# Kernel tuning notes

Measured on AMD Instinct MI355X. Metric: run time of the kernel, lower is better.

Reference implementation:

```python
import jax, jax.numpy as jnp
import numpy as np

K = 16  # neighbors, incl. self


def setup_inputs() -> dict:
    key = jax.random.key(0)
    ks = jax.random.split(key, 16)
    N, C = 8192, 256  # points, channels (inter_channels == in_channels == C)
    s = 0.05
    inp = {
        'coords': jax.random.uniform(ks[0], (N, 3), dtype=jnp.float32) * 100.0,
        'feats': jax.random.normal(ks[1], (N, C), dtype=jnp.float32),
        'theta_w': jax.random.normal(ks[2], (C, C), dtype=jnp.float32) * s,
        'theta_b': jax.random.normal(ks[3], (C,), dtype=jnp.float32) * s,
        'phi_w': jax.random.normal(ks[4], (C, C), dtype=jnp.float32) * s,
        'phi_b': jax.random.normal(ks[5], (C,), dtype=jnp.float32) * s,
        'g_w': jax.random.normal(ks[6], (C, C), dtype=jnp.float32) * s,
        'g_b': jax.random.normal(ks[7], (C,), dtype=jnp.float32) * s,
        'pe1_w1': jax.random.normal(ks[8], (3, C), dtype=jnp.float32) * s,
        'pe1_b1': jax.random.normal(ks[9], (C,), dtype=jnp.float32) * s,
        'pe1_w2': jax.random.normal(ks[10], (C, C), dtype=jnp.float32) * s,
        'pe1_b2': jax.random.normal(ks[11], (C,), dtype=jnp.float32) * s,
        'W_w': jax.random.normal(ks[12], (C, C), dtype=jnp.float32) * s,
        'W_b': jax.random.normal(ks[13], (C,), dtype=jnp.float32) * s,
    }
    return inp


def reference(coords, feats, theta_w, theta_b, phi_w, phi_b, g_w, g_b,
              pe1_w1, pe1_b1, pe1_w2, pe1_b2, W_w, W_b):
    C = feats.shape[-1]
    # KNN (squared dists, includes self as nearest) == pytorch3d knn_points
    sq = jnp.sum(coords * coords, axis=-1)  # [N]
    d2 = sq[:, None] + sq[None, :] - 2.0 * (coords @ coords.T)  # [N,N]
    _, idx = jax.lax.top_k(-d2, K)  # [N,K] sorted by ascending distance

    nn_coords = coords[idx]            # [N,K,3] knn gather
    nn_feats = feats[idx]              # [N,K,C]

    theta_f = feats @ theta_w + theta_b          # [N,C]
    phi_f = nn_feats @ phi_w + phi_b             # [N,K,C]

    delta_coords = nn_coords - coords[:, None, :]  # [N,K,3]
    # pe1 MLP; NOTE: original code uses pe1 for both pe1 and pe2 (shared)
    pe = jax.nn.relu(delta_coords @ pe1_w1 + pe1_b1) @ pe1_w2 + pe1_b2  # [N,K,C]

    delta_features = (pe * (theta_f[:, None, :] - phi_f) + pe) / jnp.sqrt(jnp.float32(C))
    sim = jax.nn.softmax(delta_features, axis=1)  # softmax over K neighbors

    g_feats = nn_feats @ g_w + g_b               # [N,K,C]
    y = jnp.sum(sim * g_feats, axis=1)           # [N,C]

    # W (1x1 Minkowski conv == per-point linear) + residual
    return y @ W_w + W_b + feats
```

## Files before the change

### kernel.cpp

```cpp
#include <hip/hip_runtime.h>

typedef __bf16 bf16_t;
typedef bf16_t bf16x8 __attribute__((ext_vector_type(8)));
typedef bf16_t bf16x4 __attribute__((ext_vector_type(4)));
typedef bf16_t bf16x2 __attribute__((ext_vector_type(2)));
typedef float f32x4 __attribute__((ext_vector_type(4)));
typedef unsigned long long u64;

#define N_PTS 8192
#define C_DIM 256
#define K_NN 16

#define GRID_G    16
#define GRID_NC   (GRID_G * GRID_G * GRID_G)
#define GRID_CELL 6.25f
#define GRID_INV  0.16f

#define CAST_NBLK 2048
#define PREPW_NBLK 320
__global__ __launch_bounds__(256) void prep_kernel(
    const float* __restrict__ feats, bf16_t* __restrict__ fb,
    const float* __restrict__ w0, const float* __restrict__ w1,
    const float* __restrict__ w2, const float* __restrict__ w3,
    const float* __restrict__ w4, bf16_t* __restrict__ wt_base,
    int* __restrict__ cellCount, int* __restrict__ gcount) {
    const int b = blockIdx.x;
    const int t = threadIdx.x;

    if (b < CAST_NBLK) {
        int i = (b * 256 + t) * 4;
        float4 v = *(const float4*)(feats + i);
        bf16x4 o;
        o[0] = (bf16_t)v.x; o[1] = (bf16_t)v.y; o[2] = (bf16_t)v.z; o[3] = (bf16_t)v.w;
        *(bf16x4*)(fb + i) = o;
    } else if (b < CAST_NBLK + PREPW_NBLK) {
        int pb = b - CAST_NBLK;
        int m = pb >> 6;
        int bx = pb & 63;
        const float* src = (m == 0) ? w0 : (m == 1) ? w1 : (m == 2) ? w2 : (m == 3) ? w3 : w4;
        bf16_t* dst = wt_base + m * (C_DIM * C_DIM);
#pragma unroll
        for (int i = 0; i < 4; ++i) {
            int o = bx * 1024 + i * 256 + t;
            int tkb = o >> 9;
            int rem = o & 511;
            int lm = rem >> 5;
            int r = rem & 31;
            int k = (tkb & 7) * 32 + r;
            int n = (tkb >> 3) * 16 + lm;
            dst[o] = (bf16_t)src[k * C_DIM + n];
        }
    } else {
        int zb = b - CAST_NBLK - PREPW_NBLK;
        cellCount[zb * 256 + t] = 0;
        if (zb == 0 && t == 0) *gcount = 0;
    }
}

__global__ __launch_bounds__(256) void grid_count_kernel(const float* __restrict__ coords,
                                                         int* __restrict__ cellCount,
                                                         int* __restrict__ cid) {
    int i = blockIdx.x * 256 + threadIdx.x;
    float x = coords[3 * i + 0], y = coords[3 * i + 1], z = coords[3 * i + 2];
    int cx = (int)(x * GRID_INV); if (cx > GRID_G - 1) cx = GRID_G - 1;
    int cy = (int)(y * GRID_INV); if (cy > GRID_G - 1) cy = GRID_G - 1;
    int cz = (int)(z * GRID_INV); if (cz > GRID_G - 1) cz = GRID_G - 1;
    int c = (cx * GRID_G + cy) * GRID_G + cz;
    cid[i] = c;
    atomicAdd(&cellCount[c], 1);
}

__global__ __launch_bounds__(256) void grid_scan_kernel(const int* __restrict__ cellCount,
                                                        int* __restrict__ cellStart,
                                                        int* __restrict__ cellPtr) {
    __shared__ int part[256];
    int t = threadIdx.x;
    int base = t * 16;
    int v[16];
    int sum = 0;
#pragma unroll
    for (int i = 0; i < 16; ++i) { v[i] = cellCount[base + i]; sum += v[i]; }
    part[t] = sum;
    __syncthreads();
    for (int off = 1; off < 256; off <<= 1) {
        int x = (t >= off) ? part[t - off] : 0;
        __syncthreads();
        part[t] += x;
        __syncthreads();
    }
    int acc = part[t] - sum;
#pragma unroll
    for (int i = 0; i < 16; ++i) {
        cellStart[base + i] = acc;
        cellPtr[base + i] = acc;
        acc += v[i];
    }
    if (t == 255) cellStart[GRID_NC] = acc;
}

__global__ __launch_bounds__(256) void grid_scatter_kernel(
    const float* __restrict__ coords, const int* __restrict__ cid, int* __restrict__ cellPtr,
    float* __restrict__ sx, float* __restrict__ sy, float* __restrict__ sz,
    float* __restrict__ ssq, int* __restrict__ sidx) {
    int i = blockIdx.x * 256 + threadIdx.x;
    int c = cid[i];
    int pos = atomicAdd(&cellPtr[c], 1);
    float x = coords[3 * i + 0], y = coords[3 * i + 1], z = coords[3 * i + 2];
    sx[pos] = x; sy[pos] = y; sz[pos] = z;
    ssq[pos] = __fadd_rn(__fadd_rn(__fmul_rn(x, x), __fmul_rn(y, y)), __fmul_rn(z, z));
    sidx[pos] = i;
}

__global__ __launch_bounds__(256) void knn_grid_kernel(
    const float* __restrict__ coords, const int* __restrict__ cellStart,
    const float* __restrict__ sx, const float* __restrict__ sy,
    const float* __restrict__ sz, const float* __restrict__ ssq,
    const int* __restrict__ sidx,
    int* __restrict__ idx_out, int* __restrict__ glist, int* __restrict__ gcount) {
    const int tid = threadIdx.x;
    const int wave = tid >> 6, lane = tid & 63;
    const int q = blockIdx.x * 4 + wave;

    __shared__ int segBase[4][25];
    __shared__ int segPref[4][26];
    __shared__ u64 cand[4][256];
    __shared__ int cnt[4];

    if (lane == 0) cnt[wave] = 0;

    const float qx = coords[3 * q + 0], qy = coords[3 * q + 1], qz = coords[3 * q + 2];
    const float sqi = __fadd_rn(__fadd_rn(__fmul_rn(qx, qx), __fmul_rn(qy, qy)),
                                __fmul_rn(qz, qz));

    int cx = (int)(qx * GRID_INV); if (cx > GRID_G - 1) cx = GRID_G - 1;
    int cy = (int)(qy * GRID_INV); if (cy > GRID_G - 1) cy = GRID_G - 1;
    int cz = (int)(qz * GRID_INV); if (cz > GRID_G - 1) cz = GRID_G - 1;
    int wx0 = cx - 2; if (wx0 < 0) wx0 = 0;
    int wx1 = cx + 2; if (wx1 > GRID_G - 1) wx1 = GRID_G - 1;
    int wy0 = cy - 2; if (wy0 < 0) wy0 = 0;
    int wy1 = cy + 2; if (wy1 > GRID_G - 1) wy1 = GRID_G - 1;
    int wz0 = cz - 2; if (wz0 < 0) wz0 = 0;
    int wz1 = cz + 2; if (wz1 > GRID_G - 1) wz1 = GRID_G - 1;

    const float INF = __int_as_float(0x7f800000);
    float rc = INF;
    if (wx0 > 0)          rc = fminf(rc, qx - (float)wx0 * GRID_CELL);
    if (wx1 < GRID_G - 1) rc = fminf(rc, (float)(wx1 + 1) * GRID_CELL - qx);
    if (wy0 > 0)          rc = fminf(rc, qy - (float)wy0 * GRID_CELL);
    if (wy1 < GRID_G - 1) rc = fminf(rc, (float)(wy1 + 1) * GRID_CELL - qy);
    if (wz0 > 0)          rc = fminf(rc, qz - (float)wz0 * GRID_CELL);
    if (wz1 < GRID_G - 1) rc = fminf(rc, (float)(wz1 + 1) * GRID_CELL - qz);
    float rc2 = rc * rc * 0.9999f;

    int nx = wx1 - wx0 + 1, nyc = wy1 - wy0 + 1;
    int ns = nx * nyc;
    if (lane < ns) {
        int scx = wx0 + lane / nyc;
        int scy = wy0 + lane % nyc;
        int b = (scx * GRID_G + scy) * GRID_G;
        int s0 = cellStart[b + wz0];
        int s1 = cellStart[b + wz1 + 1];
        segBase[wave][lane] = s0;
        segPref[wave][lane] = s1 - s0;
    }
    __syncthreads();
    if (lane == 0) {
        int acc = 0;
        for (int s = 0; s < ns; ++s) { int l = segPref[wave][s]; segPref[wave][s] = acc; acc += l; }
        segPref[wave][ns] = acc;
    }
    __syncthreads();

    const int M = segPref[wave][ns];
    bool flag = (M < K_NN);

    float lmin = INF;
    {
        int s = 0;
        for (int t = lane; t < M; t += 64) {
            while (t >= segPref[wave][s + 1]) ++s;
            int pos = segBase[wave][s] + (t - segPref[wave][s]);
            float x = sx[pos], y = sy[pos], z = sz[pos], sj = ssq[pos];
            float dot = __fmaf_rn(z, qz, __fmaf_rn(y, qy, __fmul_rn(x, qx)));
            float d2 = __fsub_rn(__fadd_rn(sqi, sj), __fmul_rn(2.0f, dot));
            lmin = fminf(lmin, d2);
        }
    }
    float g = fminf(lmin, __shfl_xor(lmin, 1));
    g = fminf(g, __shfl_xor(g, 2));
    float tau = fmaxf(g, __shfl_xor(g, 4));
    tau = fmaxf(tau, __shfl_xor(tau, 8));
    tau = fmaxf(tau, __shfl_xor(tau, 16));
    tau = fmaxf(tau, __shfl_xor(tau, 32));

    {
        int s = 0;
        for (int t = lane; t < M; t += 64) {
            while (t >= segPref[wave][s + 1]) ++s;
            int pos = segBase[wave][s] + (t - segPref[wave][s]);
            float x = sx[pos], y = sy[pos], z = sz[pos], sj = ssq[pos];
            float dot = __fmaf_rn(z, qz, __fmaf_rn(y, qy, __fmul_rn(x, qx)));
            float d2 = __fsub_rn(__fadd_rn(sqi, sj), __fmul_rn(2.0f, dot));
            if (d2 <= tau) {
                unsigned u = __float_as_uint(d2);
                u = (u & 0x80000000u) ? ~u : (u | 0x80000000u);
                int slot = atomicAdd(&cnt[wave], 1);
                if (slot < 256)
                    cand[wave][slot] = (((u64)u) << 32) | (unsigned)sidx[pos];
            }
        }
    }
    __syncthreads();

    int m = cnt[wave];
    if (m > 256) { flag = true; m = 256; }
    u64 k0 = ~0ull, k1 = ~0ull, k2 = ~0ull, k3 = ~0ull;
    if (lane < m) k0 = cand[wave][lane];
    if (lane + 64 < m) k1 = cand[wave][lane + 64];
    if (lane + 128 < m) k2 = cand[wave][lane + 128];
    if (lane + 192 < m) k3 = cand[wave][lane + 192];
    u64 lm2 = k0; int li = 0;
    if (k1 < lm2) { lm2 = k1; li = 1; }
    if (k2 < lm2) { lm2 = k2; li = 2; }
    if (k3 < lm2) { lm2 = k3; li = 3; }
    int keep = 0;
    u64 last = ~0ull;
#pragma unroll 1
    for (int r = 0; r < 16; ++r) {
        u64 w = lm2;
#pragma unroll
        for (int off = 1; off < 64; off <<= 1) {
            u64 o = __shfl_xor(w, off);
            w = (o < w) ? o : w;
        }
        if (lane == r) keep = (int)(unsigned)(w & 0xffffffffull);
        last = w;
        if (lm2 == w) {
            if (li == 0) k0 = ~0ull;
            else if (li == 1) k1 = ~0ull;
            else if (li == 2) k2 = ~0ull;
            else k3 = ~0ull;
            lm2 = k0; li = 0;
            if (k1 < lm2) { lm2 = k1; li = 1; }
            if (k2 < lm2) { lm2 = k2; li = 2; }
            if (k3 < lm2) { lm2 = k3; li = 3; }
        }
    }

    if (!flag) {
        unsigned ou = (unsigned)(last >> 32);
        unsigned db = (ou & 0x80000000u) ? (ou ^ 0x80000000u) : ~ou;
        float d16 = __uint_as_float(db);
        if (d16 >= rc2) flag = true;
    }
    if (flag && lane == 0) {
        int sl = atomicAdd(gcount, 1);
        glist[sl] = q;
    }
    if (lane < 16) idx_out[q * K_NN + lane] = keep;
}

__global__ __launch_bounds__(256) void knn_fallback_kernel(const float* __restrict__ coords,
                                                           const int* __restrict__ glist,
                                                           const int* __restrict__ gcount,
                                                           int* __restrict__ idx_out) {
    const int count = *gcount;
    const int n0 = blockIdx.x * 4;
    if (n0 >= count) return;

    const int tid = threadIdx.x;
    const int wave = tid >> 6, lane = tid & 63;
    __shared__ float red16[4][16];
    __shared__ u64 cand[4][256];
    __shared__ int cnt[4];
    __shared__ int qids[4];

    if (tid < 4) {
        cnt[tid] = 0;
        int slot = n0 + tid;
        qids[tid] = glist[slot < count ? slot : count - 1];
    }
    __syncthreads();

    float qx[4], qy[4], qz[4], sqi[4];
#pragma unroll
    for (int q = 0; q < 4; ++q) {
        int id = qids[q];
        qx[q] = coords[3 * id + 0];
        qy[q] = coords[3 * id + 1];
        qz[q] = coords[3 * id + 2];
        sqi[q] = __fadd_rn(__fadd_rn(__fmul_rn(qx[q], qx[q]), __fmul_rn(qy[q], qy[q])),
                           __fmul_rn(qz[q], qz[q]));
    }

    const float INF = __int_as_float(0x7f800000);
    const float* cp = coords + tid * 96;

    float lmin[4] = {INF, INF, INF, INF};
#pragma unroll
    for (int c = 0; c < 4; ++c) {
        float buf[24];
#pragma unroll
        for (int v = 0; v < 6; ++v)
            *(float4*)(buf + v * 4) = *(const float4*)(cp + c * 24 + v * 4);
#pragma unroll
        for (int p = 0; p < 8; ++p) {
            float x = buf[3 * p + 0], y = buf[3 * p + 1], z = buf[3 * p + 2];
            float sqj = __fadd_rn(__fadd_rn(__fmul_rn(x, x), __fmul_rn(y, y)),
                                  __fmul_rn(z, z));
#pragma unroll
            for (int q = 0; q < 4; ++q) {
                float dot = __fmaf_rn(z, qz[q], __fmaf_rn(y, qy[q], __fmul_rn(x, qx[q])));
                float d2 = __fsub_rn(__fadd_rn(sqi[q], sqj), __fmul_rn(2.0f, dot));
                lmin[q] = fminf(lmin[q], d2);
            }
        }
    }

#pragma unroll
    for (int q = 0; q < 4; ++q) {
        float g = lmin[q];
        g = fminf(g, __shfl_xor(g, 1));
        g = fminf(g, __shfl_xor(g, 2));
        g = fminf(g, __shfl_xor(g, 4));
        g = fminf(g, __shfl_xor(g, 8));
        if ((lane & 15) == 0) red16[q][wave * 4 + (lane >> 4)] = g;
    }
    __syncthreads();

    float tau[4];
#pragma unroll
    for (int q = 0; q < 4; ++q) {
        float t = red16[q][0];
#pragma unroll
        for (int i = 1; i < 16; ++i) t = fmaxf(t, red16[q][i]);
        tau[q] = t;
    }

#pragma unroll
    for (int c = 0; c < 4; ++c) {
        float buf[24];
#pragma unroll
        for (int v = 0; v < 6; ++v)
            *(float4*)(buf + v * 4) = *(const float4*)(cp + c * 24 + v * 4);
#pragma unroll
        for (int p = 0; p < 8; ++p) {
            float x = buf[3 * p + 0], y = buf[3 * p + 1], z = buf[3 * p + 2];
            float sqj = __fadd_rn(__fadd_rn(__fmul_rn(x, x), __fmul_rn(y, y)),
                                  __fmul_rn(z, z));
            int j = tid * 32 + c * 8 + p;
#pragma unroll
            for (int q = 0; q < 4; ++q) {
                float dot = __fmaf_rn(z, qz[q], __fmaf_rn(y, qy[q], __fmul_rn(x, qx[q])));
                float d2 = __fsub_rn(__fadd_rn(sqi[q], sqj), __fmul_rn(2.0f, dot));
                if (d2 <= tau[q]) {
                    unsigned u = __float_as_uint(d2);
                    u = (u & 0x80000000u) ? ~u : (u | 0x80000000u);
                    int slot = atomicAdd(&cnt[q], 1);
                    if (slot < 256)
                        cand[q][slot] = (((u64)u) << 32) | (unsigned)j;
                }
            }
        }
    }
    __syncthreads();

    int m = cnt[wave]; if (m > 256) m = 256;
    u64 k0 = ~0ull, k1 = ~0ull, k2 = ~0ull, k3 = ~0ull;
    if (lane < m) k0 = cand[wave][lane];
    if (lane + 64 < m) k1 = cand[wave][lane + 64];
    if (lane + 128 < m) k2 = cand[wave][lane + 128];
    if (lane + 192 < m) k3 = cand[wave][lane + 192];
    u64 lm2 = k0; int li = 0;
    if (k1 < lm2) { lm2 = k1; li = 1; }
    if (k2 < lm2) { lm2 = k2; li = 2; }
    if (k3 < lm2) { lm2 = k3; li = 3; }
    int keep = 0;
#pragma unroll 1
    for (int r = 0; r < 16; ++r) {
        u64 w = lm2;
#pragma unroll
        for (int off = 1; off < 64; off <<= 1) {
            u64 o = __shfl_xor(w, off);
            w = (o < w) ? o : w;
        }
        if (lane == r) keep = (int)(unsigned)(w & 0xffffffffull);
        if (lm2 == w) {
            if (li == 0) k0 = ~0ull;
            else if (li == 1) k1 = ~0ull;
            else if (li == 2) k2 = ~0ull;
            else k3 = ~0ull;
            lm2 = k0; li = 0;
            if (k1 < lm2) { lm2 = k1; li = 1; }
            if (k2 < lm2) { lm2 = k2; li = 2; }
            if (k3 < lm2) { lm2 = k3; li = 3; }
        }
    }
    if (lane < 16) idx_out[qids[wave] * K_NN + lane] = keep;
}

__global__ __launch_bounds__(256, 2) void proj_kernel(
    const bf16_t* __restrict__ fb, const bf16_t* __restrict__ wt_base,
    const float* __restrict__ tb, const float* __restrict__ pb, const float* __restrict__ gb,
    float* __restrict__ T, bf16_t* __restrict__ PG) {
    const int sel = blockIdx.y;
    const bf16_t* Wt = wt_base + sel * (C_DIM * C_DIM);
    const float* bias = (sel == 0) ? tb : (sel == 1) ? pb : gb;
    const int wave = threadIdx.x >> 6, lane = threadIdx.x & 63;
    const int q = lane >> 4, lm = lane & 15;
    const int m0 = blockIdx.x * 64;

    bf16x8 bfr[4][8];
#pragma unroll
    for (int ti = 0; ti < 4; ++ti)
#pragma unroll
        for (int kb = 0; kb < 8; ++kb)
            bfr[ti][kb] = *(const bf16x8*)(Wt + (((wave * 4 + ti) * 8 + kb) << 9) + lm * 32 + q * 8);

    float bv[4];
#pragma unroll
    for (int ti = 0; ti < 4; ++ti) bv[ti] = bias[(wave * 4 + ti) * 16 + lm];

#pragma unroll
    for (int p = 0; p < 4; ++p) {
        const bf16_t* arow = fb + (m0 + p * 16 + lm) * C_DIM + q * 8;
        bf16x8 a[8];
#pragma unroll
        for (int kb = 0; kb < 8; ++kb) a[kb] = *(const bf16x8*)(arow + kb * 32);
        f32x4 acc[4];
#pragma unroll
        for (int ti = 0; ti < 4; ++ti) acc[ti] = (f32x4){0.f, 0.f, 0.f, 0.f};
#pragma unroll
        for (int ti = 0; ti < 4; ++ti)
#pragma unroll
            for (int kb = 0; kb < 8; ++kb)
                acc[ti] = __builtin_amdgcn_mfma_f32_16x16x32_bf16(a[kb], bfr[ti][kb], acc[ti], 0, 0, 0);

#pragma unroll
        for (int ti = 0; ti < 4; ++ti) {
            int c = (wave * 4 + ti) * 16 + lm;
#pragma unroll
            for (int r = 0; r < 4; ++r) {
                float v = acc[ti][r] + bv[ti];
                int off = (m0 + p * 16 + q * 4 + r) * C_DIM + c;
                if (sel == 0) T[off] = v;
                else if (sel == 1) PG[2 * off] = (bf16_t)v;
                else PG[2 * off + 1] = (bf16_t)v;
            }
        }
    }
}

#define HPAD 264
#define P_BLK 8
#define HROWS (P_BLK * 16)
__global__ __launch_bounds__(256, 3) void pe2_fused_kernel(
    const float* __restrict__ coords, const int* __restrict__ idx,
    const float* __restrict__ T, const bf16_t* __restrict__ PG,
    const float* __restrict__ w1, const float* __restrict__ b1, const float* __restrict__ b2,
    const bf16_t* __restrict__ Wt2, bf16_t* __restrict__ yb) {
    __shared__ __align__(16) bf16_t hbuf[2][16 * HPAD];
    __shared__ float dxyz[HROWS][3];
    __shared__ int idxl[HROWS];
    const int tid = threadIdx.x;
    const int p0 = blockIdx.x * P_BLK;
    const int half = blockIdx.y;
    const int wave = tid >> 6, lane = tid & 63;
    const int q = lane >> 4, lm = lane & 15;

    bf16x8 bfr[2][8];
#pragma unroll
    for (int ti = 0; ti < 2; ++ti)
#pragma unroll
        for (int kb = 0; kb < 8; ++kb)
            bfr[ti][kb] = *(const bf16x8*)(Wt2 + ((((half * 8 + wave * 2 + ti) * 8 + kb)) << 9) + lm * 32 + q * 8);
    float b2c[2];
#pragma unroll
    for (int ti = 0; ti < 2; ++ti) b2c[ti] = b2[(half * 8 + wave * 2 + ti) * 16 + lm];

    if (tid < HROWS) {
        int n = p0 + (tid >> 4);
        int j = idx[n * K_NN + (tid & 15)];
        idxl[tid] = j;
        dxyz[tid][0] = coords[3 * j + 0] - coords[3 * n + 0];
        dxyz[tid][1] = coords[3 * j + 1] - coords[3 * n + 1];
        dxyz[tid][2] = coords[3 * j + 2] - coords[3 * n + 2];
    }
    __syncthreads();

    const float wx = w1[tid], wy = w1[C_DIM + tid], wz = w1[2 * C_DIM + tid], bb = b1[tid];

    {
#pragma unroll
        for (int r = 0; r < 16; ++r) {
            float pre = dxyz[r][0] * wx + dxyz[r][1] * wy + dxyz[r][2] * wz + bb;
            hbuf[0][r * HPAD + tid] = (bf16_t)fmaxf(pre, 0.0f);
        }
    }
    __syncthreads();

#pragma unroll 1
    for (int lp = 0; lp < P_BLK; ++lp) {
        const int n = p0 + lp;
        const int cur = lp & 1;

        int jr[4];
#pragma unroll
        for (int r = 0; r < 4; ++r) jr[r] = idxl[lp * 16 + q * 4 + r];
        bf16x2 pg[2][4];
        float Tn[2];
#pragma unroll
        for (int ti = 0; ti < 2; ++ti) {
            int c = (half * 8 + wave * 2 + ti) * 16 + lm;
            Tn[ti] = T[n * C_DIM + c];
#pragma unroll
            for (int r = 0; r < 4; ++r)
                pg[ti][r] = *(const bf16x2*)(PG + 2 * (jr[r] * C_DIM + c));
        }

        if (lp + 1 < P_BLK) {
            int rb = (lp + 1) * 16;
#pragma unroll
            for (int r = 0; r < 16; ++r) {
                float pre = dxyz[rb + r][0] * wx + dxyz[rb + r][1] * wy + dxyz[rb + r][2] * wz + bb;
                hbuf[cur ^ 1][r * HPAD + tid] = (bf16_t)fmaxf(pre, 0.0f);
            }
        }

        const bf16_t* hrow = &hbuf[cur][lm * HPAD + q * 8];
        f32x4 acc[2];
        acc[0] = (f32x4){0.f, 0.f, 0.f, 0.f};
        acc[1] = (f32x4){0.f, 0.f, 0.f, 0.f};
#pragma unroll
        for (int kb = 0; kb < 8; ++kb) {
            bf16x8 a = *(const bf16x8*)(hrow + kb * 32);
            acc[0] = __builtin_amdgcn_mfma_f32_16x16x32_bf16(a, bfr[0][kb], acc[0], 0, 0, 0);
            acc[1] = __builtin_amdgcn_mfma_f32_16x16x32_bf16(a, bfr[1][kb], acc[1], 0, 0, 0);
        }

#pragma unroll
        for (int ti = 0; ti < 2; ++ti) {
            int c = (half * 8 + wave * 2 + ti) * 16 + lm;
            float df[4];
#pragma unroll
            for (int r = 0; r < 4; ++r) {
                float pe = acc[ti][r] + b2c[ti];
                df[r] = (pe * (Tn[ti] - (float)pg[ti][r][0]) + pe) * 0.0625f;
            }
            float mx = fmaxf(fmaxf(df[0], df[1]), fmaxf(df[2], df[3]));
            mx = fmaxf(mx, __shfl_xor(mx, 16));
            mx = fmaxf(mx, __shfl_xor(mx, 32));
            float e[4], s = 0.f;
#pragma unroll
            for (int r = 0; r < 4; ++r) { e[r] = __expf(df[r] - mx); s += e[r]; }
            s += __shfl_xor(s, 16);
            s += __shfl_xor(s, 32);
            float inv = 1.0f / s;
            float y = 0.f;
#pragma unroll
            for (int r = 0; r < 4; ++r) y += e[r] * inv * (float)pg[ti][r][1];
            y += __shfl_xor(y, 16);
            y += __shfl_xor(y, 32);
            if (q == 0) yb[n * C_DIM + c] = (bf16_t)y;
        }
        __syncthreads();
    }
}

__global__ __launch_bounds__(256, 2) void final_kernel(
    const bf16_t* __restrict__ yb, const bf16_t* __restrict__ Wt,
    const float* __restrict__ Wb, const float* __restrict__ feats,
    float* __restrict__ out) {
    const int wave = threadIdx.x >> 6, lane = threadIdx.x & 63;
    const int q = lane >> 4, lm = lane & 15;
    const int m0 = blockIdx.x * 64;

    bf16x8 bfr[4][8];
#pragma unroll
    for (int ti = 0; ti < 4; ++ti)
#pragma unroll
        for (int kb = 0; kb < 8; ++kb)
            bfr[ti][kb] = *(const bf16x8*)(Wt + (((wave * 4 + ti) * 8 + kb) << 9) + lm * 32 + q * 8);
    float bv[4];
#pragma unroll
    for (int ti = 0; ti < 4; ++ti) bv[ti] = Wb[(wave * 4 + ti) * 16 + lm];

#pragma unroll
    for (int p = 0; p < 4; ++p) {
        const bf16_t* arow = yb + (m0 + p * 16 + lm) * C_DIM + q * 8;
        bf16x8 a[8];
#pragma unroll
        for (int kb = 0; kb < 8; ++kb) a[kb] = *(const bf16x8*)(arow + kb * 32);
        f32x4 acc[4];
#pragma unroll
        for (int ti = 0; ti < 4; ++ti) acc[ti] = (f32x4){0.f, 0.f, 0.f, 0.f};
#pragma unroll
        for (int ti = 0; ti < 4; ++ti)
#pragma unroll
            for (int kb = 0; kb < 8; ++kb)
                acc[ti] = __builtin_amdgcn_mfma_f32_16x16x32_bf16(a[kb], bfr[ti][kb], acc[ti], 0, 0, 0);

#pragma unroll
        for (int ti = 0; ti < 4; ++ti) {
            int c = (wave * 4 + ti) * 16 + lm;
#pragma unroll
            for (int r = 0; r < 4; ++r) {
                int off = (m0 + p * 16 + q * 4 + r) * C_DIM + c;
                out[off] = acc[ti][r] + bv[ti] + feats[off];
            }
        }
    }
}

extern "C" void kernel_launch(void* const* d_in, const int* in_sizes, int n_in,
                              void* d_out, int out_size, void* d_ws, size_t ws_size,
                              hipStream_t stream) {
    const float* coords = (const float*)d_in[0];
    const float* feats  = (const float*)d_in[1];
    const float* theta_w = (const float*)d_in[2];
    const float* theta_b = (const float*)d_in[3];
    const float* phi_w   = (const float*)d_in[4];
    const float* phi_b   = (const float*)d_in[5];
    const float* g_w     = (const float*)d_in[6];
    const float* g_b     = (const float*)d_in[7];
    const float* pe1_w1  = (const float*)d_in[8];
    const float* pe1_b1  = (const float*)d_in[9];
    const float* pe1_w2  = (const float*)d_in[10];
    const float* pe1_b2  = (const float*)d_in[11];
    const float* W_w     = (const float*)d_in[12];
    const float* W_b     = (const float*)d_in[13];
    float* out = (float*)d_out;

    char* w = (char*)d_ws;
    size_t off = 0;
    int* idx = (int*)(w + off);        off += (size_t)N_PTS * K_NN * 4;
    bf16_t* fb = (bf16_t*)(w + off);   off += (size_t)N_PTS * C_DIM * 2;
    bf16_t* wt = (bf16_t*)(w + off);   off += (size_t)5 * C_DIM * C_DIM * 2;
    float* T = (float*)(w + off);      off += (size_t)N_PTS * C_DIM * 4;
    bf16_t* PG = (bf16_t*)(w + off);   off += (size_t)N_PTS * C_DIM * 4;
    bf16_t* yb = (bf16_t*)(w + off);   off += (size_t)N_PTS * C_DIM * 2;
    int* cid       = (int*)(w + off);  off += (size_t)N_PTS * 4;
    int* cellCount = (int*)(w + off);  off += (size_t)GRID_NC * 4;
    int* cellStart = (int*)(w + off);  off += (size_t)(GRID_NC + 1) * 4;
    int* cellPtr   = (int*)(w + off);  off += (size_t)GRID_NC * 4;
    float* sxp = (float*)(w + off);    off += (size_t)N_PTS * 4;
    float* syp = (float*)(w + off);    off += (size_t)N_PTS * 4;
    float* szp = (float*)(w + off);    off += (size_t)N_PTS * 4;
    float* ssqp = (float*)(w + off);   off += (size_t)N_PTS * 4;
    int* sidxp = (int*)(w + off);      off += (size_t)N_PTS * 4;
    int* glist = (int*)(w + off);      off += (size_t)N_PTS * 4;
    int* gcount = (int*)(w + off);     off += 256;
    (void)ws_size; (void)in_sizes; (void)n_in; (void)out_size;

    prep_kernel<<<CAST_NBLK + PREPW_NBLK + 16, 256, 0, stream>>>(
        feats, fb, theta_w, phi_w, g_w, pe1_w2, W_w, wt, cellCount, gcount);

    grid_count_kernel<<<N_PTS / 256, 256, 0, stream>>>(coords, cellCount, cid);
    grid_scan_kernel<<<1, 256, 0, stream>>>(cellCount, cellStart, cellPtr);
    grid_scatter_kernel<<<N_PTS / 256, 256, 0, stream>>>(coords, cid, cellPtr,
                                                         sxp, syp, szp, ssqp, sidxp);
    knn_grid_kernel<<<N_PTS / 4, 256, 0, stream>>>(coords, cellStart, sxp, syp, szp,
                                                   ssqp, sidxp, idx, glist, gcount);
    knn_fallback_kernel<<<N_PTS / 4, 256, 0, stream>>>(coords, glist, gcount, idx);

    proj_kernel<<<dim3(N_PTS / 64, 3), 256, 0, stream>>>(fb, wt, theta_b, phi_b, g_b, T, PG);
    pe2_fused_kernel<<<dim3(N_PTS / P_BLK, 2), 256, 0, stream>>>(coords, idx, T, PG,
                                                                 pe1_w1, pe1_b1, pe1_b2,
                                                                 wt + 3 * C_DIM * C_DIM, yb);
    final_kernel<<<N_PTS / 64, 256, 0, stream>>>(yb, wt + 4 * C_DIM * C_DIM, W_b, feats, out);
}
```

Before: 209.7 us.

## Split projection GEMMs by column half and merge pe2 halves into 512-thread blocks

The projection and final GEMM kernels now split output columns across two blocks (each wave holds 2 weight tiles instead of 4), which doubles the grid and lowers register pressure. The pe2 fused kernel merges its two column halves into one 512-thread block, so the hidden-layer ReLU buffer and neighbour indices are computed once per point block and shared by all 256 columns instead of being computed twice. The costs are more blocks that each reload the A rows, and larger pe2 blocks that may limit occupancy.

```diff
diff --git a/kernel.cpp b/kernel.cpp
--- a/kernel.cpp
+++ b/kernel.cpp
@@ -404,41 +404,40 @@
     const float* __restrict__ tb, const float* __restrict__ pb, const float* __restrict__ gb,
     float* __restrict__ T, bf16_t* __restrict__ PG) {
     const int sel = blockIdx.y;
+    const int half = blockIdx.z;
     const bf16_t* Wt = wt_base + sel * (C_DIM * C_DIM);
     const float* bias = (sel == 0) ? tb : (sel == 1) ? pb : gb;
     const int wave = threadIdx.x >> 6, lane = threadIdx.x & 63;
     const int q = lane >> 4, lm = lane & 15;
     const int m0 = blockIdx.x * 64;
 
-    bf16x8 bfr[4][8];
-#pragma unroll
-    for (int ti = 0; ti < 4; ++ti)
+    bf16x8 bfr[2][8];
+#pragma unroll
+    for (int ti = 0; ti < 2; ++ti)
 #pragma unroll
         for (int kb = 0; kb < 8; ++kb)
-            bfr[ti][kb] = *(const bf16x8*)(Wt + (((wave * 4 + ti) * 8 + kb) << 9) + lm * 32 + q * 8);
-
-    float bv[4];
-#pragma unroll
-    for (int ti = 0; ti < 4; ++ti) bv[ti] = bias[(wave * 4 + ti) * 16 + lm];
+            bfr[ti][kb] = *(const bf16x8*)(Wt + (((half * 8 + wave * 2 + ti) * 8 + kb) << 9) + lm * 32 + q * 8);
+
+    float bv[2];
+#pragma unroll
+    for (int ti = 0; ti < 2; ++ti) bv[ti] = bias[(half * 8 + wave * 2 + ti) * 16 + lm];
 
 #pragma unroll
     for (int p = 0; p < 4; ++p) {
         const bf16_t* arow = fb + (m0 + p * 16 + lm) * C_DIM + q * 8;
-        bf16x8 a[8];
-#pragma unroll
-        for (int kb = 0; kb < 8; ++kb) a[kb] = *(const bf16x8*)(arow + kb * 32);
-        f32x4 acc[4];
-#pragma unroll
-        for (int ti = 0; ti < 4; ++ti) acc[ti] = (f32x4){0.f, 0.f, 0.f, 0.f};
-#pragma unroll
-        for (int ti = 0; ti < 4; ++ti)
-#pragma unroll
-            for (int kb = 0; kb < 8; ++kb)
-                acc[ti] = __builtin_amdgcn_mfma_f32_16x16x32_bf16(a[kb], bfr[ti][kb], acc[ti], 0, 0, 0);
-
-#pragma unroll
-        for (int ti = 0; ti < 4; ++ti) {
-            int c = (wave * 4 + ti) * 16 + lm;
+        f32x4 acc[2];
+        acc[0] = (f32x4){0.f, 0.f, 0.f, 0.f};
+        acc[1] = (f32x4){0.f, 0.f, 0.f, 0.f};
+#pragma unroll
+        for (int kb = 0; kb < 8; ++kb) {
+            bf16x8 a = *(const bf16x8*)(arow + kb * 32);
+            acc[0] = __builtin_amdgcn_mfma_f32_16x16x32_bf16(a, bfr[0][kb], acc[0], 0, 0, 0);
+            acc[1] = __builtin_amdgcn_mfma_f32_16x16x32_bf16(a, bfr[1][kb], acc[1], 0, 0, 0);
+        }
+
+#pragma unroll
+        for (int ti = 0; ti < 2; ++ti) {
+            int c = (half * 8 + wave * 2 + ti) * 16 + lm;
 #pragma unroll
             for (int r = 0; r < 4; ++r) {
                 float v = acc[ti][r] + bv[ti];
@@ -454,7 +453,7 @@
 #define HPAD 264
 #define P_BLK 8
 #define HROWS (P_BLK * 16)
-__global__ __launch_bounds__(256, 3) void pe2_fused_kernel(
+__global__ __launch_bounds__(512, 4) void pe2_fused_kernel(
     const float* __restrict__ coords, const int* __restrict__ idx,
     const float* __restrict__ T, const bf16_t* __restrict__ PG,
     const float* __restrict__ w1, const float* __restrict__ b1, const float* __restrict__ b2,
@@ -464,7 +463,6 @@
     __shared__ int idxl[HROWS];
     const int tid = threadIdx.x;
     const int p0 = blockIdx.x * P_BLK;
-    const int half = blockIdx.y;
     const int wave = tid >> 6, lane = tid & 63;
     const int q = lane >> 4, lm = lane & 15;
 
@@ -473,10 +471,10 @@
     for (int ti = 0; ti < 2; ++ti)
 #pragma unroll
         for (int kb = 0; kb < 8; ++kb)
-            bfr[ti][kb] = *(const bf16x8*)(Wt2 + ((((half * 8 + wave * 2 + ti) * 8 + kb)) << 9) + lm * 32 + q * 8);
+            bfr[ti][kb] = *(const bf16x8*)(Wt2 + (((wave * 2 + ti) * 8 + kb) << 9) + lm * 32 + q * 8);
     float b2c[2];
 #pragma unroll
-    for (int ti = 0; ti < 2; ++ti) b2c[ti] = b2[(half * 8 + wave * 2 + ti) * 16 + lm];
+    for (int ti = 0; ti < 2; ++ti) b2c[ti] = b2[(wave * 2 + ti) * 16 + lm];
 
     if (tid < HROWS) {
         int n = p0 + (tid >> 4);
@@ -488,14 +486,15 @@
     }
     __syncthreads();
 
-    const float wx = w1[tid], wy = w1[C_DIM + tid], wz = w1[2 * C_DIM + tid], bb = b1[tid];
-
-    {
-#pragma unroll
-        for (int r = 0; r < 16; ++r) {
-            float pre = dxyz[r][0] * wx + dxyz[r][1] * wy + dxyz[r][2] * wz + bb;
-            hbuf[0][r * HPAD + tid] = (bf16_t)fmaxf(pre, 0.0f);
-        }
+    const int hc = tid & 255;
+    const int rh = (tid >> 8) * 8;
+    const float wx = w1[hc], wy = w1[C_DIM + hc], wz = w1[2 * C_DIM + hc], bb = b1[hc];
+
+#pragma unroll
+    for (int r = 0; r < 8; ++r) {
+        int row = rh + r;
+        float pre = dxyz[row][0] * wx + dxyz[row][1] * wy + dxyz[row][2] * wz + bb;
+        hbuf[0][row * HPAD + hc] = (bf16_t)fmaxf(pre, 0.0f);
     }
     __syncthreads();
 
@@ -511,7 +510,7 @@
         float Tn[2];
 #pragma unroll
         for (int ti = 0; ti < 2; ++ti) {
-            int c = (half * 8 + wave * 2 + ti) * 16 + lm;
+            int c = (wave * 2 + ti) * 16 + lm;
             Tn[ti] = T[n * C_DIM + c];
 #pragma unroll
             for (int r = 0; r < 4; ++r)
@@ -521,9 +520,11 @@
         if (lp + 1 < P_BLK) {
             int rb = (lp + 1) * 16;
 #pragma unroll
-            for (int r = 0; r < 16; ++r) {
-                float pre = dxyz[rb + r][0] * wx + dxyz[rb + r][1] * wy + dxyz[rb + r][2] * wz + bb;
-                hbuf[cur ^ 1][r * HPAD + tid] = (bf16_t)fmaxf(pre, 0.0f);
+            for (int r = 0; r < 8; ++r) {
+                int row = rh + r;
+                float pre = dxyz[rb + row][0] * wx + dxyz[rb + row][1] * wy
+                          + dxyz[rb + row][2] * wz + bb;
+                hbuf[cur ^ 1][row * HPAD + hc] = (bf16_t)fmaxf(pre, 0.0f);
             }
         }
 
@@ -540,7 +541,7 @@
 
 #pragma unroll
         for (int ti = 0; ti < 2; ++ti) {
-            int c = (half * 8 + wave * 2 + ti) * 16 + lm;
+            int c = (wave * 2 + ti) * 16 + lm;
             float df[4];
 #pragma unroll
             for (int r = 0; r < 4; ++r) {
@@ -574,35 +575,34 @@
     const int wave = threadIdx.x >> 6, lane = threadIdx.x & 63;
     const int q = lane >> 4, lm = lane & 15;
     const int m0 = blockIdx.x * 64;
-
-    bf16x8 bfr[4][8];
-#pragma unroll
-    for (int ti = 0; ti < 4; ++ti)
+    const int half = blockIdx.y;
+
+    bf16x8 bfr[2][8];
+#pragma unroll
+    for (int ti = 0; ti < 2; ++ti)
 #pragma unroll
         for (int kb = 0; kb < 8; ++kb)
-            bfr[ti][kb] = *(const bf16x8*)(Wt + (((wave * 4 + ti) * 8 + kb) << 9) + lm * 32 + q * 8);
-    float bv[4];
-#pragma unroll
-    for (int ti = 0; ti < 4; ++ti) bv[ti] = Wb[(wave * 4 + ti) * 16 + lm];
+            bfr[ti][kb] = *(const bf16x8*)(Wt + (((half * 8 + wave * 2 + ti) * 8 + kb) << 9) + lm * 32 + q * 8);
+    float bv[2];
+#pragma unroll
+    for (int ti = 0; ti < 2; ++ti) bv[ti] = Wb[(half * 8 + wave * 2 + ti) * 16 + lm];
 
 #pragma unroll
     for (int p = 0; p < 4; ++p) {
         const bf16_t* arow = yb + (m0 + p * 16 + lm) * C_DIM + q * 8;
-        bf16x8 a[8];
-#pragma unroll
-        for (int kb = 0; kb < 8; ++kb) a[kb] = *(const bf16x8*)(arow + kb * 32);
-        f32x4 acc[4];
-#pragma unroll
-        for (int ti = 0; ti < 4; ++ti) acc[ti] = (f32x4){0.f, 0.f, 0.f, 0.f};
-#pragma unroll
-        for (int ti = 0; ti < 4; ++ti)
-#pragma unroll
-            for (int kb = 0; kb < 8; ++kb)
-                acc[ti] = __builtin_amdgcn_mfma_f32_16x16x32_bf16(a[kb], bfr[ti][kb], acc[ti], 0, 0, 0);
-
-#pragma unroll
-        for (int ti = 0; ti < 4; ++ti) {
-            int c = (wave * 4 + ti) * 16 + lm;
+        f32x4 acc[2];
+        acc[0] = (f32x4){0.f, 0.f, 0.f, 0.f};
+        acc[1] = (f32x4){0.f, 0.f, 0.f, 0.f};
+#pragma unroll
+        for (int kb = 0; kb < 8; ++kb) {
+            bf16x8 a = *(const bf16x8*)(arow + kb * 32);
+            acc[0] = __builtin_amdgcn_mfma_f32_16x16x32_bf16(a, bfr[0][kb], acc[0], 0, 0, 0);
+            acc[1] = __builtin_amdgcn_mfma_f32_16x16x32_bf16(a, bfr[1][kb], acc[1], 0, 0, 0);
+        }
+
+#pragma unroll
+        for (int ti = 0; ti < 2; ++ti) {
+            int c = (half * 8 + wave * 2 + ti) * 16 + lm;
 #pragma unroll
             for (int r = 0; r < 4; ++r) {
                 int off = (m0 + p * 16 + q * 4 + r) * C_DIM + c;
@@ -663,9 +663,10 @@
                                                    ssqp, sidxp, idx, glist, gcount);
     knn_fallback_kernel<<<N_PTS / 4, 256, 0, stream>>>(coords, glist, gcount, idx);
 
-    proj_kernel<<<dim3(N_PTS / 64, 3), 256, 0, stream>>>(fb, wt, theta_b, phi_b, g_b, T, PG);
-    pe2_fused_kernel<<<dim3(N_PTS / P_BLK, 2), 256, 0, stream>>>(coords, idx, T, PG,
-                                                                 pe1_w1, pe1_b1, pe1_b2,
-                                                                 wt + 3 * C_DIM * C_DIM, yb);
-    final_kernel<<<N_PTS / 64, 256, 0, stream>>>(yb, wt + 4 * C_DIM * C_DIM, W_b, feats, out);
-}
+    proj_kernel<<<dim3(N_PTS / 64, 3, 2), 256, 0, stream>>>(fb, wt, theta_b, phi_b, g_b, T, PG);
+    pe2_fused_kernel<<<N_PTS / P_BLK, 512, 0, stream>>>(coords, idx, T, PG,
+                                                        pe1_w1, pe1_b1, pe1_b2,
+                                                        wt + 3 * C_DIM * C_DIM, yb);
+    final_kernel<<<dim3(N_PTS / 64, 2), 256, 0, stream>>>(yb, wt + 4 * C_DIM * C_DIM,
+                                                          W_b, feats, out);
+}
```

Result: faster. 202.5 us (-3.4%).
